# Kernel tuning notes

Hardware: AMD Instinct MI355X
Metric: run time of the kernel (lower is better)

Reference implementation:

```python
import jax, jax.numpy as jnp
import numpy as np

GAMMA = 1.0

def setup_inputs() -> dict:
    key = jax.random.key(0)
    kq, kk, kv = jax.random.split(key, 3)
    B, N, M, D = 4, 2048, 2048, 128
    q = jax.random.normal(kq, (B, N, D), dtype=jnp.float32)
    k = jax.random.normal(kk, (B, M, D), dtype=jnp.float32)
    v = jax.random.normal(kv, (B, M, D), dtype=jnp.float32)
    return {"q": q, "k": k, "v": v}

def reference(q, k, v):
    # RBF attention: weights = softmax(-gamma * ||q_i - k_j||^2, axis=-1)
    # dist2 via expansion ||q||^2 + ||k||^2 - 2 q.k (same math as broadcast-subtract,
    # avoids materializing the [B,N,M,D] tensor the torch code builds).
    q2 = jnp.sum(q * q, axis=-1)                    # [B,N]
    k2 = jnp.sum(k * k, axis=-1)                    # [B,M]
    qk = jnp.einsum('bnd,bmd->bnm', q, k)           # [B,N,M]
    dist2 = q2[:, :, None] + k2[:, None, :] - 2.0 * qk
    weights = jax.nn.softmax(-GAMMA * dist2, axis=-1)  # [B,N,M]
    return jnp.einsum('bnm,bmd->bnd', weights, v)      # [B,N,D]
```

## Files before the change

### kernel.cpp

```cpp
#include <hip/hip_runtime.h>
#include <hip/hip_bf16.h>

#define B_ 4
#define N_ 2048
#define M_ 2048
#define D_ 128
#define QBLK 128
#define NTHREADS 256
#define KVBLK 64
#define NTILES 32
#define TILE_BYTES 16384
#define SPLIT_MAX 8
#define SCALE2LOG 2.885390081777927f
#define LOG2E 1.4426950408889634f
#define DEFER_THR 11.5424f

typedef __attribute__((ext_vector_type(8))) short short8;
typedef __attribute__((ext_vector_type(8))) _Float16 half8;
typedef __attribute__((ext_vector_type(16))) float floatx16;
typedef __attribute__((ext_vector_type(4))) unsigned int u32x4;
typedef unsigned short u16;
typedef unsigned int u32;

__device__ __forceinline__ u16 f2bf(float x) {
  u32 u = __builtin_bit_cast(u32, x);
  u32 r = (u + 0x7FFFu + ((u >> 16) & 1u)) >> 16;
  return (u16)r;
}
__device__ __forceinline__ float bf2f(u16 h) {
  u32 u = ((u32)h) << 16;
  return __builtin_bit_cast(float, u);
}
__device__ __forceinline__ u32 cvtpkh(float a, float b) {
  u32 r;
  asm("v_cvt_pkrtz_f16_f32 %0, %1, %2" : "=v"(r) : "v"(a), "v"(b));
  return r;
}

#define GLOAD16(src, dst)                                                     \
  __builtin_amdgcn_global_load_lds(                                           \
      (const __attribute__((address_space(1))) void*)(src),                   \
      (__attribute__((address_space(3))) void*)(dst), 16, 0, 0)

__global__ __launch_bounds__(256) void prep_kernel(
    const float* __restrict__ k, const float* __restrict__ v,
    u16* __restrict__ kf_g, u16* __restrict__ vt_g, float* __restrict__ k2_g)
{
  __shared__ u16 T[64][136];
  int tid = threadIdx.x;
  if (blockIdx.x < 512) {
    int gid = blockIdx.x * 256 + tid;
    int row_g = gid >> 4;
    int j = gid & 15;
    const float* kp = k + (size_t)row_g * D_ + j * 8;
    float4 a = *(const float4*)kp;
    float4 c = *(const float4*)(kp + 4);
    float xs[8] = {a.x, a.y, a.z, a.w, c.x, c.y, c.z, c.w};
    half8 kf;
    float ss = 0.f;
    #pragma unroll
    for (int e = 0; e < 8; ++e) {
      ss += xs[e] * xs[e];
      kf[e] = (_Float16)(SCALE2LOG * xs[e]);
    }
    ss += __shfl_xor(ss, 1);
    ss += __shfl_xor(ss, 2);
    ss += __shfl_xor(ss, 4);
    ss += __shfl_xor(ss, 8);
    if (j == 0) k2_g[row_g] = ss * LOG2E;
    int m = row_g & (M_ - 1);
    int b = row_g >> 11;
    int tile = m >> 6, r = m & 63;
    size_t base = ((size_t)b * NTILES + tile) * TILE_BYTES;
    u32 off = (u32)(r * 256 + j * 16) ^ ((u32)(r & 7) << 4);
    *(half8*)((char*)kf_g + base + off) = kf;
  } else {
    int blk = blockIdx.x - 512;
    int b = blk >> 5, tile = blk & 31;
    const float* vp = v + ((size_t)b * M_ + tile * 64) * D_;
    #pragma unroll
    for (int p = 0; p < 8; ++p) {
      int idx = p * 256 + tid;
      int r = idx >> 5, c4 = idx & 31;
      float4 vv = *(const float4*)(vp + (size_t)r * D_ + c4 * 4);
      T[r][c4 * 4 + 0] = __builtin_bit_cast(u16, (_Float16)vv.x);
      T[r][c4 * 4 + 1] = __builtin_bit_cast(u16, (_Float16)vv.y);
      T[r][c4 * 4 + 2] = __builtin_bit_cast(u16, (_Float16)vv.z);
      T[r][c4 * 4 + 3] = __builtin_bit_cast(u16, (_Float16)vv.w);
    }
    __syncthreads();
    size_t base = ((size_t)b * NTILES + tile) * TILE_BYTES;
    #pragma unroll
    for (int p = 0; p < 4; ++p) {
      int idx = p * 256 + tid;
      int d = idx >> 3, rb = idx & 7;
      short8 s;
      #pragma unroll
      for (int i = 0; i < 8; ++i) s[i] = (short)T[rb * 8 + i][d];
      u32 off = (u32)(d * 128 + rb * 16) ^ ((u32)(d & 7) << 4);
      *(short8*)((char*)vt_g + base + off) = s;
    }
  }
}

__global__ __launch_bounds__(NTHREADS, 2) void rbf_attn_kernel(
    const float* __restrict__ q, const u16* __restrict__ kf_g,
    const u16* __restrict__ vt_g, const float* __restrict__ k2_g,
    float* __restrict__ out, u16* __restrict__ Opart,
    float* __restrict__ mpart, float* __restrict__ lpart,
    int nsplit, int tiles_per_split)
{
  __shared__ __align__(16) u16 KfL[2][64 * 128];
  __shared__ __align__(16) u16 VtL[2][128 * 64];
  __shared__ __align__(16) float k2L[2][64];

  const int tid = threadIdx.x;
  const int w = tid >> 6;
  const int lane = tid & 63;
  const int qlc = lane & 31;
  const int h = lane >> 5;

  int b, qi, sp;
  {
    int gid = blockIdx.x;
    if (nsplit >= 2) {
      int xcd = gid & 7, slot = gid >> 3;
      int gpx = nsplit >> 1;
      int group = xcd * gpx + (slot >> 4);
      qi = slot & 15;
      b = group & 3;
      sp = group >> 2;
    } else {
      qi = gid & 15;
      b = gid >> 4;
      sp = 0;
    }
  }
  const int qt = qi;
  const int q0 = qt * QBLK;
  const int kt0 = sp * tiles_per_split, kt1 = kt0 + tiles_per_split;

  const char* kf_b = (const char*)kf_g + (size_t)b * NTILES * TILE_BYTES;
  const char* vt_b = (const char*)vt_g + (size_t)b * NTILES * TILE_BYTES;
  const float* k2_b = k2_g + (size_t)b * M_;
  const int so = tid * 16;

  #define STAGE(buf, kt)                                                      \
    do {                                                                      \
      const char* kh_ = kf_b + (size_t)(kt) * TILE_BYTES;                     \
      const char* vt_ = vt_b + (size_t)(kt) * TILE_BYTES;                     \
      char* dk = (char*)KfL[buf];                                             \
      char* dv = (char*)VtL[buf];                                             \
      _Pragma("unroll")                                                       \
      for (int c = 0; c < 4; ++c)                                             \
        GLOAD16(kh_ + c * 4096 + so, dk + c * 4096 + w * 1024);               \
      _Pragma("unroll")                                                       \
      for (int c = 0; c < 4; ++c)                                             \
        GLOAD16(vt_ + c * 4096 + so, dv + c * 4096 + w * 1024);               \
      if (tid < 16)                                                           \
        GLOAD16((const char*)(k2_b + (kt) * KVBLK) + tid * 16,                \
                (char*)k2L[buf]);                                             \
    } while (0)

  STAGE(0, kt0);

  half8 Qf[8];
  {
    const float* qp = q + ((size_t)b * N_ + q0 + w * 32 + qlc) * D_ + h * 8;
    #pragma unroll
    for (int s = 0; s < 8; ++s) {
      float4 a = *(const float4*)(qp + s * 16);
      float4 c = *(const float4*)(qp + s * 16 + 4);
      Qf[s][0] = (_Float16)a.x; Qf[s][1] = (_Float16)a.y;
      Qf[s][2] = (_Float16)a.z; Qf[s][3] = (_Float16)a.w;
      Qf[s][4] = (_Float16)c.x; Qf[s][5] = (_Float16)c.y;
      Qf[s][6] = (_Float16)c.z; Qf[s][7] = (_Float16)c.w;
    }
  }

  floatx16 o[4];
  #pragma unroll
  for (int dt = 0; dt < 4; ++dt) o[dt] = (floatx16)0.0f;
  float mrun = -1e30f, lrun = 0.f;

  asm volatile("s_waitcnt vmcnt(0)" ::: "memory");
  __syncthreads();

  int pb = 0;
  for (int kt = kt0; kt < kt1; ++kt) {
    if (kt + 1 < kt1) STAGE(pb ^ 1, kt + 1);

    const char* Kb = (const char*)KfL[pb];
    const char* Vb = (const char*)VtL[pb];
    const float* k2p = k2L[pb];

    floatx16 accS0 = (floatx16)0.0f, accS1 = (floatx16)0.0f;
    __builtin_amdgcn_s_setprio(1);
    #pragma unroll
    for (int s = 0; s < 8; ++s) {
      {
        int row = qlc;
        u32 off = ((u32)(row * 256 + s * 32 + h * 16)) ^ ((u32)(row & 7) << 4);
        half8 af = *(const half8*)(Kb + off);
        accS0 = __builtin_amdgcn_mfma_f32_32x32x16_f16(af, Qf[s], accS0, 0, 0, 0);
      }
      {
        int row = 32 + qlc;
        u32 off = ((u32)(row * 256 + s * 32 + h * 16)) ^ ((u32)(row & 7) << 4);
        half8 af = *(const half8*)(Kb + off);
        accS1 = __builtin_amdgcn_mfma_f32_32x32x16_f16(af, Qf[s], accS1, 0, 0, 0);
      }
    }
    __builtin_amdgcn_s_setprio(0);

    float mx = -3e38f;
    #pragma unroll
    for (int ct = 0; ct < 2; ++ct) {
      #pragma unroll
      for (int g = 0; g < 4; ++g) {
        float4 kq = *(const float4*)&k2p[32 * ct + 8 * g + 4 * h];
        if (ct == 0) {
          accS0[4 * g + 0] -= kq.x; accS0[4 * g + 1] -= kq.y;
          accS0[4 * g + 2] -= kq.z; accS0[4 * g + 3] -= kq.w;
          mx = fmaxf(mx, fmaxf(fmaxf(accS0[4 * g], accS0[4 * g + 1]),
                               fmaxf(accS0[4 * g + 2], accS0[4 * g + 3])));
        } else {
          accS1[4 * g + 0] -= kq.x; accS1[4 * g + 1] -= kq.y;
          accS1[4 * g + 2] -= kq.z; accS1[4 * g + 3] -= kq.w;
          mx = fmaxf(mx, fmaxf(fmaxf(accS1[4 * g], accS1[4 * g + 1]),
                               fmaxf(accS1[4 * g + 2], accS1[4 * g + 3])));
        }
      }
    }
    mx = fmaxf(mx, __shfl_xor(mx, 32));
    if (!__all(mx - mrun <= DEFER_THR)) {
      float mnew = fmaxf(mrun, mx);
      float scl = exp2f(mrun - mnew);
      mrun = mnew;
      lrun *= scl;
      #pragma unroll
      for (int i = 0; i < 16; ++i) {
        o[0][i] *= scl; o[1][i] *= scl; o[2][i] *= scl; o[3][i] *= scl;
      }
    }
    float ls = 0.f;
    u32 W[2][4][2];
    #pragma unroll
    for (int ct = 0; ct < 2; ++ct) {
      #pragma unroll
      for (int g = 0; g < 4; ++g) {
        float p0, p1, p2, p3;
        if (ct == 0) {
          p0 = exp2f(accS0[4 * g + 0] - mrun); p1 = exp2f(accS0[4 * g + 1] - mrun);
          p2 = exp2f(accS0[4 * g + 2] - mrun); p3 = exp2f(accS0[4 * g + 3] - mrun);
        } else {
          p0 = exp2f(accS1[4 * g + 0] - mrun); p1 = exp2f(accS1[4 * g + 1] - mrun);
          p2 = exp2f(accS1[4 * g + 2] - mrun); p3 = exp2f(accS1[4 * g + 3] - mrun);
        }
        ls += (p0 + p1) + (p2 + p3);
        W[ct][g][0] = cvtpkh(p0, p1);
        W[ct][g][1] = cvtpkh(p2, p3);
      }
    }
    ls += __shfl_xor(ls, 32);
    lrun += ls;

    u32 X[2][4][2];
    #pragma unroll
    for (int ct = 0; ct < 2; ++ct)
      #pragma unroll
      for (int g = 0; g < 4; ++g) {
        X[ct][g][0] = __shfl_xor(W[ct][g][0], 32);
        X[ct][g][1] = __shfl_xor(W[ct][g][1], 32);
      }

    const bool h0 = (h == 0);
    __builtin_amdgcn_s_setprio(1);
    #pragma unroll
    for (int s2 = 0; s2 < 4; ++s2) {
      const int ct = s2 >> 1, e = s2 & 1;
      u32 w0 = h0 ? W[ct][2 * e][0] : X[ct][2 * e + 1][0];
      u32 w1 = h0 ? W[ct][2 * e][1] : X[ct][2 * e + 1][1];
      u32 w2 = h0 ? X[ct][2 * e][0] : W[ct][2 * e + 1][0];
      u32 w3 = h0 ? X[ct][2 * e][1] : W[ct][2 * e + 1][1];
      half8 pf = __builtin_bit_cast(half8, (u32x4){w0, w1, w2, w3});
      #pragma unroll
      for (int dt = 0; dt < 4; ++dt) {
        int row = dt * 32 + qlc;
        u32 off = ((u32)(row * 128 + s2 * 32 + h * 16)) ^ ((u32)(row & 7) << 4);
        half8 af = *(const half8*)(Vb + off);
        o[dt] = __builtin_amdgcn_mfma_f32_32x32x16_f16(af, pf, o[dt], 0, 0, 0);
      }
    }
    __builtin_amdgcn_s_setprio(0);

    asm volatile("s_waitcnt vmcnt(0)" ::: "memory");
    __syncthreads();
    pb ^= 1;
  }

  const int qt32 = qt * 4 + w;
  if (nsplit == 1) {
    float inv = 1.0f / lrun;
    float* ob = out + ((size_t)b * N_ + q0 + w * 32 + qlc) * D_;
    #pragma unroll
    for (int dt = 0; dt < 4; ++dt)
      #pragma unroll
      for (int r = 0; r < 16; ++r) {
        int d = dt * 32 + (r & 3) + 8 * (r >> 2) + 4 * h;
        ob[d] = o[dt][r] * inv;
      }
  } else {
    u16* ob = Opart + ((((size_t)sp * B_ + b) * (N_ / 32) + qt32) * D_) * 32;
    #pragma unroll
    for (int dt = 0; dt < 4; ++dt)
      #pragma unroll
      for (int r = 0; r < 16; ++r) {
        int d = dt * 32 + (r & 3) + 8 * (r >> 2) + 4 * h;
        ob[(size_t)d * 32 + qlc] = f2bf(o[dt][r]);
      }
    if (h == 0) {
      size_t mrow = ((size_t)sp * B_ + b) * N_ + qt32 * 32 + qlc;
      mpart[mrow] = mrun;
      lpart[mrow] = lrun;
    }
  }
}

__global__ __launch_bounds__(256) void rbf_reduce_kernel(
    const u16* __restrict__ Opart, const float* __restrict__ mpart,
    const float* __restrict__ lpart, float* __restrict__ out, int nsplit)
{
  __shared__ float T[32][136];
  const int t = threadIdx.x;
  const int qln = t & 31, dg = t >> 5;
  const int b = blockIdx.x >> 6, qt32 = blockIdx.x & 63;
  const size_t stride = (size_t)B_ * N_;
  const size_t mbase = (size_t)b * N_ + qt32 * 32 + qln;
  float mmax = -3e38f;
  for (int s = 0; s < nsplit; ++s)
    mmax = fmaxf(mmax, mpart[s * stride + mbase]);
  float acc[16];
  #pragma unroll
  for (int i = 0; i < 16; ++i) acc[i] = 0.f;
  float lsum = 0.f;
  for (int s = 0; s < nsplit; ++s) {
    float wv = exp2f(mpart[s * stride + mbase] - mmax);
    lsum += wv * lpart[s * stride + mbase];
    const u16* ob = Opart +
        ((((size_t)s * B_ + b) * (N_ / 32) + qt32) * D_ + dg * 16) * 32 + qln;
    #pragma unroll
    for (int dd = 0; dd < 16; ++dd) acc[dd] += wv * bf2f(ob[(size_t)dd * 32]);
  }
  float inv = 1.0f / lsum;
  #pragma unroll
  for (int dd = 0; dd < 16; ++dd) T[qln][dg * 16 + dd] = acc[dd] * inv;
  __syncthreads();
  const int r = t >> 3, seg = t & 7;
  float* op = out + ((size_t)b * N_ + qt32 * 32 + r) * D_ + seg * 16;
  #pragma unroll
  for (int i = 0; i < 4; ++i) {
    float4 v4 = {T[r][seg * 16 + 4 * i], T[r][seg * 16 + 4 * i + 1],
                 T[r][seg * 16 + 4 * i + 2], T[r][seg * 16 + 4 * i + 3]};
    *(float4*)(op + 4 * i) = v4;
  }
}

extern "C" void kernel_launch(void* const* d_in, const int* in_sizes, int n_in,
                              void* d_out, int out_size, void* d_ws, size_t ws_size,
                              hipStream_t stream) {
  const float* q = (const float*)d_in[0];
  const float* k = (const float*)d_in[1];
  const float* v = (const float*)d_in[2];
  float* out = (float*)d_out;

  const size_t tileBytesAll = (size_t)B_ * NTILES * TILE_BYTES;
  u16* kf_g = (u16*)d_ws;
  u16* vt_g = (u16*)((char*)d_ws + tileBytesAll);
  float* k2_g = (float*)((char*)d_ws + 2 * tileBytesAll);
  const size_t prepBytes = 2 * tileBytesAll + (size_t)B_ * M_ * sizeof(float);

  const size_t perO = (size_t)B_ * N_ * D_ * sizeof(u16);
  const size_t perML = 2 * (size_t)B_ * N_ * sizeof(float);
  int nsplit = SPLIT_MAX;
  while (nsplit > 1 && prepBytes + (size_t)nsplit * (perO + perML) > ws_size)
    nsplit >>= 1;

  u16* Opart = (u16*)((char*)d_ws + prepBytes);
  float* mpart = (float*)((char*)d_ws + prepBytes + (size_t)nsplit * perO);
  float* lpart = mpart + (size_t)nsplit * B_ * N_;
  int tiles_per_split = NTILES / nsplit;

  prep_kernel<<<512 + B_ * NTILES, 256, 0, stream>>>(k, v, kf_g, vt_g, k2_g);

  rbf_attn_kernel<<<dim3(16 * B_ * nsplit), NTHREADS, 0, stream>>>(
      q, kf_g, vt_g, k2_g, out, Opart, mpart, lpart, nsplit, tiles_per_split);
  if (nsplit > 1) {
    rbf_reduce_kernel<<<B_ * (N_ / 32), 256, 0, stream>>>(
        Opart, mpart, lpart, out, nsplit);
  }
}
```

Before: 39.47 us.

## Double query block per workgroup to 256 rows and split reduce over D halves

Each attention workgroup now handles 256 query rows with 512 threads (8 waves), so every staged K/V tile in LDS is reused by twice as many waves and the grid has half as many blocks. The tile loader is adjusted to 2 copy iterations of 8KB per thread group. The reduce kernel is split into two blocks per 32-row group, each covering half of D, to double its parallelism. The larger blocks may lower occupancy under launch_bounds(…,2) with 512 threads, and the halved grid may underfill the CUs.

Result: no change. 38.78 us (-1.8%).

```diff
diff --git a/kernel.cpp b/kernel.cpp
--- a/kernel.cpp
+++ b/kernel.cpp
@@ -5,8 +5,8 @@
 #define N_ 2048
 #define M_ 2048
 #define D_ 128
-#define QBLK 128
-#define NTHREADS 256
+#define QBLK 256
+#define NTHREADS 512
 #define KVBLK 64
 #define NTILES 32
 #define TILE_BYTES 16384
@@ -89,7 +89,7 @@
       T[r][c4 * 4 + 3] = __builtin_bit_cast(u16, (_Float16)vv.w);
     }
     __syncthreads();
-    size_t base = ((size_t)b * NTILES + tile) * TILE_BYTES;
+    size_t base = (size_t)blk * TILE_BYTES;
     #pragma unroll
     for (int p = 0; p < 4; ++p) {
       int idx = p * 256 + tid;
@@ -110,8 +110,8 @@
     float* __restrict__ mpart, float* __restrict__ lpart,
     int nsplit, int tiles_per_split)
 {
-  __shared__ __align__(16) u16 KfL[2][64 * 128];
-  __shared__ __align__(16) u16 VtL[2][128 * 64];
+  __shared__ __align__(16) u16 KfL[2][8192];
+  __shared__ __align__(16) u16 VtL[2][8192];
   __shared__ __align__(16) float k2L[2][64];
 
   const int tid = threadIdx.x;
@@ -126,13 +126,13 @@
     if (nsplit >= 2) {
       int xcd = gid & 7, slot = gid >> 3;
       int gpx = nsplit >> 1;
-      int group = xcd * gpx + (slot >> 4);
-      qi = slot & 15;
+      int group = xcd * gpx + (slot >> 3);
+      qi = slot & 7;
       b = group & 3;
       sp = group >> 2;
     } else {
-      qi = gid & 15;
-      b = gid >> 4;
+      qi = gid & 7;
+      b = gid >> 3;
       sp = 0;
     }
   }
@@ -152,11 +152,11 @@
       char* dk = (char*)KfL[buf];                                             \
       char* dv = (char*)VtL[buf];                                             \
       _Pragma("unroll")                                                       \
-      for (int c = 0; c < 4; ++c)                                             \
-        GLOAD16(kh_ + c * 4096 + so, dk + c * 4096 + w * 1024);               \
+      for (int c = 0; c < 2; ++c)                                             \
+        GLOAD16(kh_ + c * 8192 + so, dk + c * 8192 + w * 1024);               \
       _Pragma("unroll")                                                       \
-      for (int c = 0; c < 4; ++c)                                             \
-        GLOAD16(vt_ + c * 4096 + so, dv + c * 4096 + w * 1024);               \
+      for (int c = 0; c < 2; ++c)                                             \
+        GLOAD16(vt_ + c * 8192 + so, dv + c * 8192 + w * 1024);               \
       if (tid < 16)                                                           \
         GLOAD16((const char*)(k2_b + (kt) * KVBLK) + tid * 16,                \
                 (char*)k2L[buf]);                                             \
@@ -299,7 +299,7 @@
     pb ^= 1;
   }
 
-  const int qt32 = qt * 4 + w;
+  const int qt32 = qt * 8 + w;
   if (nsplit == 1) {
     float inv = 1.0f / lrun;
     float* ob = out + ((size_t)b * N_ + q0 + w * 32 + qlc) * D_;
@@ -325,45 +325,48 @@
       lpart[mrow] = lrun;
     }
   }
+  #undef STAGE
 }
 
 __global__ __launch_bounds__(256) void rbf_reduce_kernel(
     const u16* __restrict__ Opart, const float* __restrict__ mpart,
     const float* __restrict__ lpart, float* __restrict__ out, int nsplit)
 {
-  __shared__ float T[32][136];
+  __shared__ float T2[32 * 72];
   const int t = threadIdx.x;
+  const int unit = blockIdx.x;
+  const int group = unit >> 1, dhalf = unit & 1;
+  const int b = group >> 6, qt32 = group & 63;
   const int qln = t & 31, dg = t >> 5;
-  const int b = blockIdx.x >> 6, qt32 = blockIdx.x & 63;
   const size_t stride = (size_t)B_ * N_;
   const size_t mbase = (size_t)b * N_ + qt32 * 32 + qln;
   float mmax = -3e38f;
   for (int s = 0; s < nsplit; ++s)
     mmax = fmaxf(mmax, mpart[s * stride + mbase]);
-  float acc[16];
+  float acc[8];
   #pragma unroll
-  for (int i = 0; i < 16; ++i) acc[i] = 0.f;
+  for (int i = 0; i < 8; ++i) acc[i] = 0.f;
   float lsum = 0.f;
   for (int s = 0; s < nsplit; ++s) {
     float wv = exp2f(mpart[s * stride + mbase] - mmax);
     lsum += wv * lpart[s * stride + mbase];
     const u16* ob = Opart +
-        ((((size_t)s * B_ + b) * (N_ / 32) + qt32) * D_ + dg * 16) * 32 + qln;
-    #pragma unroll
-    for (int dd = 0; dd < 16; ++dd) acc[dd] += wv * bf2f(ob[(size_t)dd * 32]);
+        ((((size_t)s * B_ + b) * (N_ / 32) + qt32) * D_ + dhalf * 64 + dg * 8) * 32 + qln;
+    #pragma unroll
+    for (int dd = 0; dd < 8; ++dd) acc[dd] += wv * bf2f(ob[(size_t)dd * 32]);
   }
   float inv = 1.0f / lsum;
   #pragma unroll
-  for (int dd = 0; dd < 16; ++dd) T[qln][dg * 16 + dd] = acc[dd] * inv;
+  for (int dd = 0; dd < 8; ++dd) T2[qln * 72 + dg * 8 + dd] = acc[dd] * inv;
   __syncthreads();
   const int r = t >> 3, seg = t & 7;
-  float* op = out + ((size_t)b * N_ + qt32 * 32 + r) * D_ + seg * 16;
-  #pragma unroll
-  for (int i = 0; i < 4; ++i) {
-    float4 v4 = {T[r][seg * 16 + 4 * i], T[r][seg * 16 + 4 * i + 1],
-                 T[r][seg * 16 + 4 * i + 2], T[r][seg * 16 + 4 * i + 3]};
-    *(float4*)(op + 4 * i) = v4;
-  }
+  float* op = out + ((size_t)b * N_ + qt32 * 32 + r) * D_ + dhalf * 64 + seg * 8;
+  float4 v0 = {T2[r * 72 + seg * 8 + 0], T2[r * 72 + seg * 8 + 1],
+               T2[r * 72 + seg * 8 + 2], T2[r * 72 + seg * 8 + 3]};
+  float4 v1 = {T2[r * 72 + seg * 8 + 4], T2[r * 72 + seg * 8 + 5],
+               T2[r * 72 + seg * 8 + 6], T2[r * 72 + seg * 8 + 7]};
+  *(float4*)op = v0;
+  *(float4*)(op + 4) = v1;
 }
 
 extern "C" void kernel_launch(void* const* d_in, const int* in_sizes, int n_in,
@@ -393,10 +396,10 @@
 
   prep_kernel<<<512 + B_ * NTILES, 256, 0, stream>>>(k, v, kf_g, vt_g, k2_g);
 
-  rbf_attn_kernel<<<dim3(16 * B_ * nsplit), NTHREADS, 0, stream>>>(
+  rbf_attn_kernel<<<dim3(8 * B_ * nsplit), NTHREADS, 0, stream>>>(
       q, kf_g, vt_g, k2_g, out, Opart, mpart, lpart, nsplit, tiles_per_split);
   if (nsplit > 1) {
-    rbf_reduce_kernel<<<B_ * (N_ / 32), 256, 0, stream>>>(
+    rbf_reduce_kernel<<<2 * B_ * (N_ / 32), 256, 0, stream>>>(
         Opart, mpart, lpart, out, nsplit);
   }
 }
```
